# Optimization experiments

Measured on AMD Instinct MI355X. Metric: run time of the kernel, lower is better.

## Reference

```python
import jax, jax.numpy as jnp
import numpy as np

ALPHA = 0.2
TAU = 0.25
NB_ITERATIONS = 10
EPS = 1e-12


def _grad2d(u):
    # forward differences with Neumann boundary (zero at last col/row)
    px = jnp.roll(u, -1, axis=3) - u
    px = px.at[..., -1].set(0.0)
    py = jnp.roll(u, -1, axis=2) - u
    py = py.at[..., -1, :].set(0.0)
    return px, py


def _div2d(px, py):
    div_x = px - jnp.roll(px, 1, axis=3)
    div_x = div_x.at[..., 0].set(px[..., 0])
    div_y = py - jnp.roll(py, 1, axis=2)
    div_y = div_y.at[..., 0, :].set(py[..., 0, :])
    return div_x + div_y


def _proj_unit_ball(px, py):
    norm = jnp.sqrt(px * px + py * py + EPS)
    scale = jnp.maximum(norm, 1.0)
    return px / scale, py / scale


def setup_inputs() -> dict:
    key = jax.random.key(0)
    z = jax.random.normal(key, (8, 64, 256, 256), dtype=jnp.float32)
    lam = jnp.asarray(0.2, dtype=jnp.float32)
    return {"z": z, "lam": lam}


def reference(z, lam):
    lam_c = jnp.clip(lam, 0.0, 1.0)  # get_lambda()
    u = jax.nn.leaky_relu(z, negative_slope=ALPHA)
    px = jnp.zeros_like(u)
    py = jnp.zeros_like(u)

    def body(carry, _):
        u, px, py = carry
        gx, gy = _grad2d(u)
        px = px + lam_c * TAU * gx
        py = py + lam_c * TAU * gy
        px, py = _proj_unit_ball(px, py)
        div_p = _div2d(px, py)
        u = jax.nn.leaky_relu(z + lam_c * div_p, negative_slope=ALPHA)
        return (u, px, py), None

    (u, px, py), _ = jax.lax.scan(body, (u, px, py), None, length=NB_ITERATIONS)
    return u
```

## Files before the change

### kernel.cpp

```cpp
#include <hip/hip_runtime.h>

namespace {

constexpr float ALPHA = 0.2f;
constexpr float TAU   = 0.25f;
constexpr int   NITER = 10;

constexpr int H = 256, W = 256;
constexpr int TILE = 64;
constexpr int HALO = 10;
constexpr int RG   = TILE + 2*HALO;
constexpr int QR   = RG / 4;
constexpr int RQ   = RG / 4;
constexpr int NTH  = RQ * QR;
constexpr int NT   = 448;

constexpr int SUR0_OFF = 0;
constexpr int SUC0_OFF = 22 * RG;
constexpr int SPY_OFF  = SUC0_OFF + RG * 22;
constexpr int SPX_OFF  = SPY_OFF + RQ * RG;
constexpr int DUMP_OFF = SPX_OFF + RG * QR;
constexpr int LDS_FLOATS = DUMP_OFF + 96;

constexpr int DUMP_SUR0 = DUMP_OFF - SUR0_OFF;
constexpr int DUMP_SUC0 = DUMP_OFF - SUC0_OFF;
constexpr int DUMP_SPY  = DUMP_OFF - SPY_OFF + 84;
constexpr int DUMP_SPX  = DUMP_OFF - SPX_OFF + 1;

typedef float v2f __attribute__((ext_vector_type(2)));

#if defined(__has_builtin)
#if __has_builtin(__builtin_amdgcn_rsqf)
#define RSQ(x) __builtin_amdgcn_rsqf(x)
#endif
#endif
#ifndef RSQ
#define RSQ(x) rsqrtf(x)
#endif

__launch_bounds__(NT, 4)
__global__ void tv_lrelu_kernel(const float* __restrict__ z,
                                const float* __restrict__ lam_p,
                                float* __restrict__ out) {
  __shared__ __align__(16) float lds[LDS_FLOATS];
  float* const su_r0 = lds + SUR0_OFF;
  float* const su_c0 = lds + SUC0_OFF;
  float* const spy   = lds + SPY_OFF;
  float* const spx   = lds + SPX_OFF;

  const float lam_c = fminf(fmaxf(lam_p[0], 0.0f), 1.0f);
  const float cg = lam_c * TAU;

  const int b   = blockIdx.x;
  const int img = b >> 4;
  const int tr  = (b >> 2) & 3;
  const int tc  = b & 3;
  const long base = (long)img * (H * W);
  const int r0 = tr * TILE - HALO;
  const int c0 = tc * TILE - HALO;

  const int tid = threadIdx.x;
  const bool act = tid < NTH;
  const int tw = act ? tid : 0;
  const int rq = tw / QR;
  const int qc = tw - rq * QR;
  const int r  = 4 * rq;
  const int gj = c0 + qc * 4;

  v2f cgx[2], nlmdx[2];
#pragma unroll
  for (int k = 0; k < 4; ++k) {
    reinterpret_cast<float*>(cgx)[k]   = (gj + k < W - 1) ? cg : 0.0f;
    reinterpret_cast<float*>(nlmdx)[k] = (gj + k > 0) ? -lam_c : 0.0f;
  }
  float cgy[4], nlmy[4];
#pragma unroll
  for (int i = 0; i < 4; ++i) {
    const int gi = r0 + r + i;
    cgy[i]  = (gi < H - 1) ? cg : 0.0f;
    nlmy[i] = (gi > 0) ? -lam_c : 0.0f;
  }

  v2f zq[4][2], u[4][2];
  v2f px[4][2] = {};
  v2f py[4][2] = {};

#pragma unroll
  for (int i = 0; i < 4; ++i) {
    const int gi = r0 + r + i;
    const bool rin = (gi >= 0) & (gi < H);
    const float* zp = z + base + (long)gi * W + gj;
    float zv[4];
#pragma unroll
    for (int k = 0; k < 4; ++k) {
      const bool cin = (gj + k >= 0) & (gj + k < W);
      zv[k] = (rin & cin) ? zp[k] : 0.0f;
    }
    zq[i][0] = (v2f){zv[0], zv[1]};
    zq[i][1] = (v2f){zv[2], zv[3]};
#pragma unroll
    for (int j = 0; j < 2; ++j)
      u[i][j] = __builtin_elementwise_max(zq[i][j], zq[i][j] * ALPHA);
  }

  const int sur0_w = act ? (rq * RG + qc * 4) : DUMP_SUR0;
  const int suc0_w = act ? (r * 22 + qc)      : DUMP_SUC0;
  const int spy_w  = act ? (rq * RG + qc * 4) : DUMP_SPY;
  const int spx_w  = act ? (r * QR + qc)      : DUMP_SPX;

  *reinterpret_cast<float4*>(&su_r0[sur0_w]) =
      make_float4(u[0][0].x, u[0][0].y, u[0][1].x, u[0][1].y);
#pragma unroll
  for (int i = 0; i < 4; ++i) su_c0[suc0_w + i * 22] = u[i][0].x;
  __syncthreads();

  for (int t = 0; t < NITER; ++t) {
    const float4 udn = *reinterpret_cast<const float4*>(&su_r0[sur0_w + RG]);
    float ur[4];
#pragma unroll
    for (int i = 0; i < 4; ++i) ur[i] = su_c0[suc0_w + i * 22 + 1];
    const v2f dn0 = {udn.x, udn.y}, dn1 = {udn.z, udn.w};

#pragma unroll
    for (int i = 0; i < 4; ++i) {
      const v2f un0 = {u[i][0].y, u[i][1].x};
      const v2f un1 = {u[i][1].y, ur[i]};
      const v2f ud0 = (i < 3) ? u[(i < 3) ? i + 1 : 0][0] : dn0;
      const v2f ud1 = (i < 3) ? u[(i < 3) ? i + 1 : 0][1] : dn1;

      px[i][0] = __builtin_elementwise_fma(cgx[0], un0 - u[i][0], px[i][0]);
      px[i][1] = __builtin_elementwise_fma(cgx[1], un1 - u[i][1], px[i][1]);
      py[i][0] = __builtin_elementwise_fma((v2f)cgy[i], ud0 - u[i][0], py[i][0]);
      py[i][1] = __builtin_elementwise_fma((v2f)cgy[i], ud1 - u[i][1], py[i][1]);
#pragma unroll
      for (int j = 0; j < 2; ++j) {
        const v2f n2 = __builtin_elementwise_fma(px[i][j], px[i][j],
                                                 py[i][j] * py[i][j]);
        const v2f m = __builtin_elementwise_max(n2, (v2f)1.0f);
        const v2f sc = {RSQ(m.x), RSQ(m.y)};
        px[i][j] *= sc;
        py[i][j] *= sc;
      }
    }
#pragma unroll
    for (int i = 0; i < 4; ++i) spx[spx_w + i * QR] = px[i][1].y;
    *reinterpret_cast<float4*>(&spy[spy_w]) =
        make_float4(py[3][0].x, py[3][0].y, py[3][1].x, py[3][1].y);
    __syncthreads();

    const float4 pyu4 = *reinterpret_cast<const float4*>(&spy[spy_w - RG]);
    float pxl[4];
#pragma unroll
    for (int i = 0; i < 4; ++i) pxl[i] = spx[spx_w + i * QR - 1];
    const v2f up0 = {pyu4.x, pyu4.y}, up1 = {pyu4.z, pyu4.w};

#pragma unroll
    for (int i = 0; i < 4; ++i) {
      const v2f pxs0 = {pxl[i], px[i][0].x};
      const v2f pxs1 = {px[i][0].y, px[i][1].x};
      const v2f pyu0 = (i == 0) ? up0 : py[(i > 0) ? i - 1 : 0][0];
      const v2f pyu1 = (i == 0) ? up1 : py[(i > 0) ? i - 1 : 0][1];

      v2f a0 = __builtin_elementwise_fma((v2f)lam_c, px[i][0] + py[i][0], zq[i][0]);
      v2f a1 = __builtin_elementwise_fma((v2f)lam_c, px[i][1] + py[i][1], zq[i][1]);
      a0 = __builtin_elementwise_fma(nlmdx[0], pxs0, a0);
      a1 = __builtin_elementwise_fma(nlmdx[1], pxs1, a1);
      a0 = __builtin_elementwise_fma((v2f)nlmy[i], pyu0, a0);
      a1 = __builtin_elementwise_fma((v2f)nlmy[i], pyu1, a1);
      u[i][0] = __builtin_elementwise_max(a0, a0 * ALPHA);
      u[i][1] = __builtin_elementwise_max(a1, a1 * ALPHA);
    }
    *reinterpret_cast<float4*>(&su_r0[sur0_w]) =
        make_float4(u[0][0].x, u[0][0].y, u[0][1].x, u[0][1].y);
#pragma unroll
    for (int i = 0; i < 4; ++i) su_c0[suc0_w + i * 22] = u[i][0].x;
    __syncthreads();
  }

  if (act) {
#pragma unroll
    for (int i = 0; i < 4; ++i) {
      const int rr = r + i;
      if (rr >= HALO && rr < HALO + TILE) {
        float* dst = out + base + (long)(r0 + rr) * W + gj;
        if (qc >= 3 && qc <= 17) {
          *reinterpret_cast<float4*>(dst) =
              make_float4(u[i][0].x, u[i][0].y, u[i][1].x, u[i][1].y);
        } else if (qc == 2 || qc == 18) {
          const float uv[4] = {u[i][0].x, u[i][0].y, u[i][1].x, u[i][1].y};
#pragma unroll
          for (int k = 0; k < 4; ++k) {
            const int cc = qc * 4 + k;
            if (cc >= HALO && cc < HALO + TILE) dst[k] = uv[k];
          }
        }
      }
    }
  }
}

}

extern "C" void kernel_launch(void* const* d_in, const int* in_sizes, int n_in,
                              void* d_out, int out_size, void* d_ws, size_t ws_size,
                              hipStream_t stream) {
  const float* z   = (const float*)d_in[0];
  const float* lam = (const float*)d_in[1];
  float* out = (float*)d_out;

  const int n_img = in_sizes[0] / (H * W);
  const int n_blocks = n_img * 16;

  tv_lrelu_kernel<<<n_blocks, NT, 0, stream>>>(z, lam, out);
}
```

Baseline: 289.4 us.

## Reload z each iteration from cache, transpose column LDS buffers, raise occupancy

Stops keeping z in registers. Each iteration reloads it from global memory through clamped-address v2f loads, which frees registers so launch bounds can ask for 6 waves-per-EU blocks instead of 4. The column-neighbour LDS buffers for u and px are transposed so each thread writes and reads one float4 instead of four scalars. Boundary row coefficients are now recomputed inline. The trade is extra global/L2 traffic every iteration, and out-of-image halo values of z are now clamped copies rather than zeros, which should only affect halo cells.

```diff
diff --git a/kernel.cpp b/kernel.cpp
--- a/kernel.cpp
+++ b/kernel.cpp
@@ -16,16 +16,16 @@
 constexpr int NT   = 448;
 
 constexpr int SUR0_OFF = 0;
-constexpr int SUC0_OFF = 22 * RG;
-constexpr int SPY_OFF  = SUC0_OFF + RG * 22;
-constexpr int SPX_OFF  = SPY_OFF + RQ * RG;
-constexpr int DUMP_OFF = SPX_OFF + RG * QR;
-constexpr int LDS_FLOATS = DUMP_OFF + 96;
-
-constexpr int DUMP_SUR0 = DUMP_OFF - SUR0_OFF;
-constexpr int DUMP_SUC0 = DUMP_OFF - SUC0_OFF;
-constexpr int DUMP_SPY  = DUMP_OFF - SPY_OFF + 84;
-constexpr int DUMP_SPX  = DUMP_OFF - SPX_OFF + 1;
+constexpr int SUC0_OFF = SUR0_OFF + 22 * RG;
+constexpr int SPY_OFF  = SUC0_OFF + 23 * RG;
+constexpr int SPX_OFF  = SPY_OFF  + 21 * RG;
+constexpr int DUMP_OFF = SPX_OFF  + 23 * RG;
+constexpr int LDS_FLOATS = DUMP_OFF + 128;
+
+constexpr int D_SUR0 = DUMP_OFF - SUR0_OFF;
+constexpr int D_SUC0 = DUMP_OFF - SUC0_OFF;
+constexpr int D_SPY  = DUMP_OFF - SPY_OFF + 84;
+constexpr int D_SPX  = DUMP_OFF - SPX_OFF + 84;
 
 typedef float v2f __attribute__((ext_vector_type(2)));
 
@@ -38,7 +38,7 @@
 #define RSQ(x) rsqrtf(x)
 #endif
 
-__launch_bounds__(NT, 4)
+__launch_bounds__(NT, 6)
 __global__ void tv_lrelu_kernel(const float* __restrict__ z,
                                 const float* __restrict__ lam_p,
                                 float* __restrict__ out) {
@@ -49,13 +49,13 @@
   float* const spx   = lds + SPX_OFF;
 
   const float lam_c = fminf(fmaxf(lam_p[0], 0.0f), 1.0f);
-  const float cg = lam_c * TAU;
+  const float cg    = lam_c * TAU;
+  const float nlam  = -lam_c;
 
   const int b   = blockIdx.x;
   const int img = b >> 4;
   const int tr  = (b >> 2) & 3;
   const int tc  = b & 3;
-  const long base = (long)img * (H * W);
   const int r0 = tr * TILE - HALO;
   const int c0 = tc * TILE - HALO;
 
@@ -65,60 +65,61 @@
   const int rq = tw / QR;
   const int qc = tw - rq * QR;
   const int r  = 4 * rq;
-  const int gj = c0 + qc * 4;
+  const int gi0 = r0 + r;
+  const int gj  = c0 + qc * 4;
 
   v2f cgx[2], nlmdx[2];
 #pragma unroll
   for (int k = 0; k < 4; ++k) {
     reinterpret_cast<float*>(cgx)[k]   = (gj + k < W - 1) ? cg : 0.0f;
-    reinterpret_cast<float*>(nlmdx)[k] = (gj + k > 0) ? -lam_c : 0.0f;
-  }
-  float cgy[4], nlmy[4];
+    reinterpret_cast<float*>(nlmdx)[k] = (gj + k > 0) ? nlam : 0.0f;
+  }
+
+  const float* zb = z + (size_t)img * (H * W);
+  const int ajlo = min(max(gj, 0), W - 2);
+  const int ajhi = min(max(gj + 2, 0), W - 2);
+  int olo[4], ohi[4];
 #pragma unroll
   for (int i = 0; i < 4; ++i) {
-    const int gi = r0 + r + i;
-    cgy[i]  = (gi < H - 1) ? cg : 0.0f;
-    nlmy[i] = (gi > 0) ? -lam_c : 0.0f;
-  }
-
-  v2f zq[4][2], u[4][2];
+    const int gic = min(max(gi0 + i, 0), H - 1);
+    olo[i] = gic * W + ajlo;
+    ohi[i] = gic * W + ajhi;
+  }
+
+  v2f u[4][2];
   v2f px[4][2] = {};
   v2f py[4][2] = {};
 
 #pragma unroll
   for (int i = 0; i < 4; ++i) {
-    const int gi = r0 + r + i;
-    const bool rin = (gi >= 0) & (gi < H);
-    const float* zp = z + base + (long)gi * W + gj;
-    float zv[4];
-#pragma unroll
-    for (int k = 0; k < 4; ++k) {
-      const bool cin = (gj + k >= 0) & (gj + k < W);
-      zv[k] = (rin & cin) ? zp[k] : 0.0f;
-    }
-    zq[i][0] = (v2f){zv[0], zv[1]};
-    zq[i][1] = (v2f){zv[2], zv[3]};
-#pragma unroll
-    for (int j = 0; j < 2; ++j)
-      u[i][j] = __builtin_elementwise_max(zq[i][j], zq[i][j] * ALPHA);
-  }
-
-  const int sur0_w = act ? (rq * RG + qc * 4) : DUMP_SUR0;
-  const int suc0_w = act ? (r * 22 + qc)      : DUMP_SUC0;
-  const int spy_w  = act ? (rq * RG + qc * 4) : DUMP_SPY;
-  const int spx_w  = act ? (r * QR + qc)      : DUMP_SPX;
-
-  *reinterpret_cast<float4*>(&su_r0[sur0_w]) =
+    const v2f zl = *reinterpret_cast<const v2f*>(zb + olo[i]);
+    const v2f zh = *reinterpret_cast<const v2f*>(zb + ohi[i]);
+    u[i][0] = __builtin_elementwise_max(zl, zl * ALPHA);
+    u[i][1] = __builtin_elementwise_max(zh, zh * ALPHA);
+  }
+
+  const int sw = act ? (rq * RG + qc * 4)       : D_SUR0;
+  const int cw = act ? ((qc + 1) * RG + rq * 4) : D_SUC0;
+  const int yw = act ? (rq * RG + qc * 4)       : D_SPY;
+  const int xw = act ? ((qc + 1) * RG + rq * 4) : D_SPX;
+
+  *reinterpret_cast<float4*>(&su_r0[sw]) =
       make_float4(u[0][0].x, u[0][0].y, u[0][1].x, u[0][1].y);
-#pragma unroll
-  for (int i = 0; i < 4; ++i) su_c0[suc0_w + i * 22] = u[i][0].x;
+  *reinterpret_cast<float4*>(&su_c0[cw]) =
+      make_float4(u[0][0].x, u[1][0].x, u[2][0].x, u[3][0].x);
   __syncthreads();
 
   for (int t = 0; t < NITER; ++t) {
-    const float4 udn = *reinterpret_cast<const float4*>(&su_r0[sur0_w + RG]);
-    float ur[4];
-#pragma unroll
-    for (int i = 0; i < 4; ++i) ur[i] = su_c0[suc0_w + i * 22 + 1];
+    v2f zl[4], zh[4];
+#pragma unroll
+    for (int i = 0; i < 4; ++i) {
+      zl[i] = *reinterpret_cast<const v2f*>(zb + olo[i]);
+      zh[i] = *reinterpret_cast<const v2f*>(zb + ohi[i]);
+    }
+
+    const float4 udn = *reinterpret_cast<const float4*>(&su_r0[sw + RG]);
+    const float4 ur4 = *reinterpret_cast<const float4*>(&su_c0[cw + RG]);
+    const float ur[4] = {ur4.x, ur4.y, ur4.z, ur4.w};
     const v2f dn0 = {udn.x, udn.y}, dn1 = {udn.z, udn.w};
 
 #pragma unroll
@@ -127,11 +128,12 @@
       const v2f un1 = {u[i][1].y, ur[i]};
       const v2f ud0 = (i < 3) ? u[(i < 3) ? i + 1 : 0][0] : dn0;
       const v2f ud1 = (i < 3) ? u[(i < 3) ? i + 1 : 0][1] : dn1;
+      const float cgy_i = (gi0 + i < H - 1) ? cg : 0.0f;
 
       px[i][0] = __builtin_elementwise_fma(cgx[0], un0 - u[i][0], px[i][0]);
       px[i][1] = __builtin_elementwise_fma(cgx[1], un1 - u[i][1], px[i][1]);
-      py[i][0] = __builtin_elementwise_fma((v2f)cgy[i], ud0 - u[i][0], py[i][0]);
-      py[i][1] = __builtin_elementwise_fma((v2f)cgy[i], ud1 - u[i][1], py[i][1]);
+      py[i][0] = __builtin_elementwise_fma((v2f)cgy_i, ud0 - u[i][0], py[i][0]);
+      py[i][1] = __builtin_elementwise_fma((v2f)cgy_i, ud1 - u[i][1], py[i][1]);
 #pragma unroll
       for (int j = 0; j < 2; ++j) {
         const v2f n2 = __builtin_elementwise_fma(px[i][j], px[i][j],
@@ -142,16 +144,15 @@
         py[i][j] *= sc;
       }
     }
-#pragma unroll
-    for (int i = 0; i < 4; ++i) spx[spx_w + i * QR] = px[i][1].y;
-    *reinterpret_cast<float4*>(&spy[spy_w]) =
+    *reinterpret_cast<float4*>(&spx[xw]) =
+        make_float4(px[0][1].y, px[1][1].y, px[2][1].y, px[3][1].y);
+    *reinterpret_cast<float4*>(&spy[yw]) =
         make_float4(py[3][0].x, py[3][0].y, py[3][1].x, py[3][1].y);
     __syncthreads();
 
-    const float4 pyu4 = *reinterpret_cast<const float4*>(&spy[spy_w - RG]);
-    float pxl[4];
-#pragma unroll
-    for (int i = 0; i < 4; ++i) pxl[i] = spx[spx_w + i * QR - 1];
+    const float4 pyu4 = *reinterpret_cast<const float4*>(&spy[yw - RG]);
+    const float4 pxl4 = *reinterpret_cast<const float4*>(&spx[xw - RG]);
+    const float pxl[4] = {pxl4.x, pxl4.y, pxl4.z, pxl4.w};
     const v2f up0 = {pyu4.x, pyu4.y}, up1 = {pyu4.z, pyu4.w};
 
 #pragma unroll
@@ -160,24 +161,26 @@
       const v2f pxs1 = {px[i][0].y, px[i][1].x};
       const v2f pyu0 = (i == 0) ? up0 : py[(i > 0) ? i - 1 : 0][0];
       const v2f pyu1 = (i == 0) ? up1 : py[(i > 0) ? i - 1 : 0][1];
-
-      v2f a0 = __builtin_elementwise_fma((v2f)lam_c, px[i][0] + py[i][0], zq[i][0]);
-      v2f a1 = __builtin_elementwise_fma((v2f)lam_c, px[i][1] + py[i][1], zq[i][1]);
+      const float nlmy_i = (gi0 + i > 0) ? nlam : 0.0f;
+
+      v2f a0 = __builtin_elementwise_fma((v2f)lam_c, px[i][0] + py[i][0], zl[i]);
+      v2f a1 = __builtin_elementwise_fma((v2f)lam_c, px[i][1] + py[i][1], zh[i]);
       a0 = __builtin_elementwise_fma(nlmdx[0], pxs0, a0);
       a1 = __builtin_elementwise_fma(nlmdx[1], pxs1, a1);
-      a0 = __builtin_elementwise_fma((v2f)nlmy[i], pyu0, a0);
-      a1 = __builtin_elementwise_fma((v2f)nlmy[i], pyu1, a1);
+      a0 = __builtin_elementwise_fma((v2f)nlmy_i, pyu0, a0);
+      a1 = __builtin_elementwise_fma((v2f)nlmy_i, pyu1, a1);
       u[i][0] = __builtin_elementwise_max(a0, a0 * ALPHA);
       u[i][1] = __builtin_elementwise_max(a1, a1 * ALPHA);
     }
-    *reinterpret_cast<float4*>(&su_r0[sur0_w]) =
+    *reinterpret_cast<float4*>(&su_r0[sw]) =
         make_float4(u[0][0].x, u[0][0].y, u[0][1].x, u[0][1].y);
-#pragma unroll
-    for (int i = 0; i < 4; ++i) su_c0[suc0_w + i * 22] = u[i][0].x;
+    *reinterpret_cast<float4*>(&su_c0[cw]) =
+        make_float4(u[0][0].x, u[1][0].x, u[2][0].x, u[3][0].x);
     __syncthreads();
   }
 
   if (act) {
+    const size_t base = (size_t)img * (H * W);
 #pragma unroll
     for (int i = 0; i < 4; ++i) {
       const int rr = r + i;
```

Measured after the change: 965.1 us. 3.33x slower.

## Use wave shuffles for column halos and recompute ghost row to drop a barrier

Applied to the files above, without the earlier changes.

Each wave of 64 lanes now holds 3 row-groups of 21 column-quads, so horizontal neighbour exchange (right u, left px) goes through lane shuffles instead of LDS. Each thread also recomputes the py value of the row above from the neighbour's u, so the mid-iteration LDS exchange and its __syncthreads are removed. The u boundary rows are double-buffered in LDS so only one barrier per iteration remains. This adds redundant projection work per thread, and shuffles at the edge lanes rely on halo columns being discarded.

```diff
diff --git a/kernel.cpp b/kernel.cpp
--- a/kernel.cpp
+++ b/kernel.cpp
@@ -11,21 +11,14 @@
 constexpr int HALO = 10;
 constexpr int RG   = TILE + 2*HALO;
 constexpr int QR   = RG / 4;
-constexpr int RQ   = RG / 4;
-constexpr int NTH  = RQ * QR;
+constexpr int GW   = 21;
 constexpr int NT   = 448;
 
-constexpr int SUR0_OFF = 0;
-constexpr int SUC0_OFF = 22 * RG;
-constexpr int SPY_OFF  = SUC0_OFF + RG * 22;
-constexpr int SPX_OFF  = SPY_OFF + RQ * RG;
-constexpr int DUMP_OFF = SPX_OFF + RG * QR;
-constexpr int LDS_FLOATS = DUMP_OFF + 96;
-
-constexpr int DUMP_SUR0 = DUMP_OFF - SUR0_OFF;
-constexpr int DUMP_SUC0 = DUMP_OFF - SUC0_OFF;
-constexpr int DUMP_SPY  = DUMP_OFF - SPY_OFF + 84;
-constexpr int DUMP_SPX  = DUMP_OFF - SPX_OFF + 1;
+constexpr int SUR0 = 0;
+constexpr int SUR3 = GW * RG;
+constexpr int BUF  = 2 * GW * RG;
+constexpr int DUMP = 2 * BUF;
+constexpr int LDS_FLOATS = DUMP + 7 * 16;
 
 typedef float v2f __attribute__((ext_vector_type(2)));
 
@@ -43,13 +36,10 @@
                                 const float* __restrict__ lam_p,
                                 float* __restrict__ out) {
   __shared__ __align__(16) float lds[LDS_FLOATS];
-  float* const su_r0 = lds + SUR0_OFF;
-  float* const su_c0 = lds + SUC0_OFF;
-  float* const spy   = lds + SPY_OFF;
-  float* const spx   = lds + SPX_OFF;
 
   const float lam_c = fminf(fmaxf(lam_p[0], 0.0f), 1.0f);
-  const float cg = lam_c * TAU;
+  const float cg    = lam_c * TAU;
+  const float nlam  = -lam_c;
 
   const int b   = blockIdx.x;
   const int img = b >> 4;
@@ -59,35 +49,40 @@
   const int r0 = tr * TILE - HALO;
   const int c0 = tc * TILE - HALO;
 
-  const int tid = threadIdx.x;
-  const bool act = tid < NTH;
-  const int tw = act ? tid : 0;
-  const int rq = tw / QR;
-  const int qc = tw - rq * QR;
+  const int tid  = threadIdx.x;
+  const int wave = tid >> 6;
+  const int lane = tid & 63;
+  const bool act = lane < 63;
+  const int lg = act ? lane / GW : 0;
+  const int qc = act ? lane - lg * GW : 0;
+  const int rq = wave * 3 + lg;
   const int r  = 4 * rq;
-  const int gj = c0 + qc * 4;
+  const int gi0 = r0 + r;
+  const int gj  = c0 + qc * 4;
+  const int laneP1 = lane + 1, laneM1 = lane - 1;
 
   v2f cgx[2], nlmdx[2];
 #pragma unroll
   for (int k = 0; k < 4; ++k) {
     reinterpret_cast<float*>(cgx)[k]   = (gj + k < W - 1) ? cg : 0.0f;
-    reinterpret_cast<float*>(nlmdx)[k] = (gj + k > 0) ? -lam_c : 0.0f;
+    reinterpret_cast<float*>(nlmdx)[k] = (gj + k > 0) ? nlam : 0.0f;
   }
   float cgy[4], nlmy[4];
 #pragma unroll
   for (int i = 0; i < 4; ++i) {
-    const int gi = r0 + r + i;
-    cgy[i]  = (gi < H - 1) ? cg : 0.0f;
-    nlmy[i] = (gi > 0) ? -lam_c : 0.0f;
-  }
+    cgy[i]  = (gi0 + i < H - 1) ? cg : 0.0f;
+    nlmy[i] = (gi0 + i > 0) ? nlam : 0.0f;
+  }
+  const float cgyG = (gi0 - 1 < H - 1) ? cg : 0.0f;
 
   v2f zq[4][2], u[4][2];
   v2f px[4][2] = {};
   v2f py[4][2] = {};
+  v2f gpx[2] = {}, gpy[2] = {};
 
 #pragma unroll
   for (int i = 0; i < 4; ++i) {
-    const int gi = r0 + r + i;
+    const int gi = gi0 + i;
     const bool rin = (gi >= 0) & (gi < H);
     const float* zp = z + base + (long)gi * W + gj;
     float zv[4];
@@ -103,24 +98,47 @@
       u[i][j] = __builtin_elementwise_max(zq[i][j], zq[i][j] * ALPHA);
   }
 
-  const int sur0_w = act ? (rq * RG + qc * 4) : DUMP_SUR0;
-  const int suc0_w = act ? (r * 22 + qc)      : DUMP_SUC0;
-  const int spy_w  = act ? (rq * RG + qc * 4) : DUMP_SPY;
-  const int spx_w  = act ? (r * QR + qc)      : DUMP_SPX;
-
-  *reinterpret_cast<float4*>(&su_r0[sur0_w]) =
+  const int wi0 = act ? (SUR0 + rq * RG + qc * 4) : (DUMP + wave * 16);
+  const int wi3 = act ? (SUR3 + rq * RG + qc * 4) : (DUMP + wave * 16 + 4);
+  const int rdn = act ? (SUR0 + (rq + 1) * RG + qc * 4) : (DUMP + wave * 16 + 8);
+  const int rup = act ? (SUR3 + (rq - 1) * RG + qc * 4) : (DUMP + wave * 16 + 8);
+  const int bofs = act ? BUF : 0;
+
+  *reinterpret_cast<float4*>(&lds[wi0]) =
       make_float4(u[0][0].x, u[0][0].y, u[0][1].x, u[0][1].y);
-#pragma unroll
-  for (int i = 0; i < 4; ++i) su_c0[suc0_w + i * 22] = u[i][0].x;
+  *reinterpret_cast<float4*>(&lds[wi3]) =
+      make_float4(u[3][0].x, u[3][0].y, u[3][1].x, u[3][1].y);
   __syncthreads();
 
   for (int t = 0; t < NITER; ++t) {
-    const float4 udn = *reinterpret_cast<const float4*>(&su_r0[sur0_w + RG]);
+    const int rb = (t & 1) ? bofs : 0;
+    const int wb = (t & 1) ? 0 : bofs;
+
+    const float4 up4 = *reinterpret_cast<const float4*>(&lds[rup + rb]);
+    const float4 dn4 = *reinterpret_cast<const float4*>(&lds[rdn + rb]);
+    const float ucor = __shfl(up4.x, laneP1);
     float ur[4];
 #pragma unroll
-    for (int i = 0; i < 4; ++i) ur[i] = su_c0[suc0_w + i * 22 + 1];
-    const v2f dn0 = {udn.x, udn.y}, dn1 = {udn.z, udn.w};
-
+    for (int i = 0; i < 4; ++i) ur[i] = __shfl(u[i][0].x, laneP1);
+
+    {
+      const v2f g0 = {up4.x, up4.y}, g1 = {up4.z, up4.w};
+      const v2f ung0 = {up4.y, up4.z}, ung1 = {up4.w, ucor};
+      gpx[0] = __builtin_elementwise_fma(cgx[0], ung0 - g0, gpx[0]);
+      gpx[1] = __builtin_elementwise_fma(cgx[1], ung1 - g1, gpx[1]);
+      gpy[0] = __builtin_elementwise_fma((v2f)cgyG, u[0][0] - g0, gpy[0]);
+      gpy[1] = __builtin_elementwise_fma((v2f)cgyG, u[0][1] - g1, gpy[1]);
+#pragma unroll
+      for (int j = 0; j < 2; ++j) {
+        const v2f n2 = __builtin_elementwise_fma(gpx[j], gpx[j], gpy[j] * gpy[j]);
+        const v2f m  = __builtin_elementwise_max(n2, (v2f)1.0f);
+        const v2f sc = {RSQ(m.x), RSQ(m.y)};
+        gpx[j] *= sc;
+        gpy[j] *= sc;
+      }
+    }
+
+    const v2f dn0 = {dn4.x, dn4.y}, dn1 = {dn4.z, dn4.w};
 #pragma unroll
     for (int i = 0; i < 4; ++i) {
       const v2f un0 = {u[i][0].y, u[i][1].x};
@@ -142,24 +160,17 @@
         py[i][j] *= sc;
       }
     }
-#pragma unroll
-    for (int i = 0; i < 4; ++i) spx[spx_w + i * QR] = px[i][1].y;
-    *reinterpret_cast<float4*>(&spy[spy_w]) =
-        make_float4(py[3][0].x, py[3][0].y, py[3][1].x, py[3][1].y);
-    __syncthreads();
-
-    const float4 pyu4 = *reinterpret_cast<const float4*>(&spy[spy_w - RG]);
+
     float pxl[4];
 #pragma unroll
-    for (int i = 0; i < 4; ++i) pxl[i] = spx[spx_w + i * QR - 1];
-    const v2f up0 = {pyu4.x, pyu4.y}, up1 = {pyu4.z, pyu4.w};
+    for (int i = 0; i < 4; ++i) pxl[i] = __shfl(px[i][1].y, laneM1);
 
 #pragma unroll
     for (int i = 0; i < 4; ++i) {
       const v2f pxs0 = {pxl[i], px[i][0].x};
       const v2f pxs1 = {px[i][0].y, px[i][1].x};
-      const v2f pyu0 = (i == 0) ? up0 : py[(i > 0) ? i - 1 : 0][0];
-      const v2f pyu1 = (i == 0) ? up1 : py[(i > 0) ? i - 1 : 0][1];
+      const v2f pyu0 = (i == 0) ? gpy[0] : py[(i > 0) ? i - 1 : 0][0];
+      const v2f pyu1 = (i == 0) ? gpy[1] : py[(i > 0) ? i - 1 : 0][1];
 
       v2f a0 = __builtin_elementwise_fma((v2f)lam_c, px[i][0] + py[i][0], zq[i][0]);
       v2f a1 = __builtin_elementwise_fma((v2f)lam_c, px[i][1] + py[i][1], zq[i][1]);
@@ -170,10 +181,11 @@
       u[i][0] = __builtin_elementwise_max(a0, a0 * ALPHA);
       u[i][1] = __builtin_elementwise_max(a1, a1 * ALPHA);
     }
-    *reinterpret_cast<float4*>(&su_r0[sur0_w]) =
+
+    *reinterpret_cast<float4*>(&lds[wi0 + wb]) =
         make_float4(u[0][0].x, u[0][0].y, u[0][1].x, u[0][1].y);
-#pragma unroll
-    for (int i = 0; i < 4; ++i) su_c0[suc0_w + i * 22] = u[i][0].x;
+    *reinterpret_cast<float4*>(&lds[wi3 + wb]) =
+        make_float4(u[3][0].x, u[3][0].y, u[3][1].x, u[3][1].y);
     __syncthreads();
   }
 
```

Result: slower. 377.0 us (+30.3%).
